# Kernel tuning notes

Hardware: AMD Instinct MI355X
Metric: run time of the kernel (lower is better)

## Reference

```python
import jax, jax.numpy as jnp
import numpy as np

B, T, D_IN = 32768, 25, 4
H = 32    # hidden_dims // 2 (per-LSTM hidden size)
HID = 64  # hidden_dims (MLP head width)
NB = 5    # number of LSTM branches
DROP = 0.4


def _lstm_layer(x_tm, Wih, Whh, b):
    # x_tm: [T, B, D] time-major. Returns all hidden states [T, B, H].
    Bn = x_tm.shape[1]
    h0 = jnp.zeros((Bn, H), x_tm.dtype)

    def step(carry, xt):
        h, c = carry
        gates = xt @ Wih.T + h @ Whh.T + b  # [B, 4H], torch gate order i,f,g,o
        i, f, g, o = jnp.split(gates, 4, axis=-1)
        c = jax.nn.sigmoid(f) * c + jax.nn.sigmoid(i) * jnp.tanh(g)
        h = jax.nn.sigmoid(o) * jnp.tanh(c)
        return (h, c), h

    (_, _), hs = jax.lax.scan(step, (h0, h0), x_tm)
    return hs


def setup_inputs() -> dict:
    key = jax.random.key(0)
    ks = jax.random.split(key, 16)
    s = 1.0 / np.sqrt(H)  # torch LSTM/Linear uniform bound scale
    u = lambda k, shape: jax.random.uniform(k, shape, jnp.float32, -s, s)
    return {
        "x": jax.random.normal(ks[0], (B, T, D_IN), jnp.float32),
        "mask": (jax.random.uniform(ks[1], (B, T, D_IN)) > DROP).astype(jnp.float32),
        # layer 0 of each of the 5 LSTMs (input D_IN -> H)
        "Wih0": u(ks[2], (NB, 4 * H, D_IN)),
        "Whh0": u(ks[3], (NB, 4 * H, H)),
        "bih0": u(ks[4], (NB, 4 * H)),
        "bhh0": u(ks[5], (NB, 4 * H)),
        # layer 1 of each of the 5 LSTMs (H -> H)
        "Wih1": u(ks[6], (NB, 4 * H, H)),
        "Whh1": u(ks[7], (NB, 4 * H, H)),
        "bih1": u(ks[8], (NB, 4 * H)),
        "bhh1": u(ks[9], (NB, 4 * H)),
        # MLP head: Linear(H->HID), GELU, Linear(HID->HID)
        "W1": u(ks[10], (HID, H)),
        "b1": u(ks[11], (HID,)),
        "W2": u(ks[12], (HID, HID)),
        "b2": u(ks[13], (HID,)),
    }


def reference(x, mask, Wih0, Whh0, bih0, bhh0, Wih1, Whh1, bih1, bhh1, W1, b1, W2, b2):
    xm = x * mask  # elementwise input dropout-mask (precomputed binary mask)
    hiddens = []
    for i in range(NB):  # fixed small structural loop over 5 distinct LSTMs
        sub = xm[:, -(i + 1) * 5 :, :]           # [B, 5*(i+1), D_IN]
        sub_tm = jnp.swapaxes(sub, 0, 1)         # time-major [t, B, D_IN]
        hs0 = _lstm_layer(sub_tm, Wih0[i], Whh0[i], bih0[i] + bhh0[i])  # [t,B,H]
        hs1 = _lstm_layer(hs0, Wih1[i], Whh1[i], bih1[i] + bhh1[i])     # [t,B,H]
        hiddens.append(hs1[-1])                  # last-layer final hidden [B,H]
    hidden = jnp.stack(hiddens, axis=1)          # [B, 5, H]
    h = jax.nn.gelu(hidden @ W1.T + b1, approximate=False)  # torch exact GELU
    out = h @ W2.T + b2                          # [B, 5, HID]
    return out
```

## Files before the change

### kernel.cpp

```cpp
#include <hip/hip_runtime.h>
#include <hip/hip_bf16.h>

#define BQ   32768
#define TT   25
#define DIN  4
#define HH   32
#define GG   128
#define NBR  5
#define HIDD 64
#define LOG2E    1.4426950408889634f
#define TWOLOG2E 2.8853900817779268f

using bfrag = __attribute__((ext_vector_type(8))) short;
using accf  = __attribute__((ext_vector_type(4))) float;

__device__ __forceinline__ float fexp2(float x){
#if __has_builtin(__builtin_amdgcn_exp2f)
  return __builtin_amdgcn_exp2f(x);
#else
  return exp2f(x);
#endif
}
__device__ __forceinline__ float frcpf(float x){
#if __has_builtin(__builtin_amdgcn_rcpf)
  return __builtin_amdgcn_rcpf(x);
#else
  return 1.0f / x;
#endif
}
__device__ __forceinline__ unsigned short fb(float f){
  unsigned u = __builtin_bit_cast(unsigned, f);
  u += 0x7fffu + ((u >> 16) & 1u);
  return (unsigned short)(u >> 16);
}
__device__ __forceinline__ bfrag pack8s(const float* p, float s){
  bfrag w;
#pragma unroll
  for (int j = 0; j < 8; ++j) w[j] = (short)fb(p[j] * s);
  return w;
}
__device__ __forceinline__ accf mma(bfrag a, bfrag b, accf c){
  return __builtin_amdgcn_mfma_f32_16x16x32_bf16(a, b, c, 0, 0, 0);
}
__device__ __forceinline__ float cellh(float iv, float fv, float gv, float ov, float& cs){
  float ei = fexp2(-iv), ef = fexp2(-fv), t = fexp2(gv);
  float r2 = frcpf(1.0f + ef);
  float r1 = frcpf((1.0f + ei) * (t + 1.0f));
  float cp = cs * r2 + ((t - 1.0f) * r1) * TWOLOG2E;
  cs = cp;
  float eo = fexp2(-ov), tc = fexp2(cp);
  float r3 = frcpf((1.0f + eo) * (tc + 1.0f));
  return (tc - 1.0f) * r3;
}

#define LDSW 4032

__global__ __launch_bounds__(64, 2) void lstm_kernel(
    const float* __restrict__ x,    const float* __restrict__ mask,
    const float* __restrict__ Wih0, const float* __restrict__ Whh0,
    const float* __restrict__ bih0, const float* __restrict__ bhh0,
    const float* __restrict__ Wih1, const float* __restrict__ Whh1,
    const float* __restrict__ bih1, const float* __restrict__ bhh1,
    const float* __restrict__ W1,   const float* __restrict__ b1,
    const float* __restrict__ W2,   const float* __restrict__ b2,
    float* __restrict__ out)
{
  __shared__ __align__(16) unsigned short smem[2 * LDSW];
  const int lane = threadIdx.x & 63;
  const int col  = lane & 15, quad = lane >> 4;
  const int tp     = blockIdx.x & 1023;
  const int branch = 4 - (int)(blockIdx.x >> 10);
  const int L = (branch + 1) * 5, t0 = TT - L;

  for (int i = lane; i < 800; i += 64) {
    int b = i / 25;
    int j = i - b * 25;
    size_t go = (size_t)(tp * 32 + b) * 100 + j * 4;
    float4 xv = *reinterpret_cast<const float4*>(x + go);
    float4 mv = *reinterpret_cast<const float4*>(mask + go);
    ushort4 sv;
    sv.x = fb(xv.x * mv.x); sv.y = fb(xv.y * mv.y);
    sv.z = fb(xv.z * mv.z); sv.w = fb(xv.w * mv.w);
    *reinterpret_cast<ushort4*>(smem + (b >> 4) * LDSW + (b & 15) * 100 + j * 4) = sv;
  }

  const float* Wih0p = Wih0 + branch * GG * DIN;
  const float* Whh0p = Whh0 + branch * GG * HH;
  const float* Wih1p = Wih1 + branch * GG * HH;
  const float* Whh1p = Whh1 + branch * GG * HH;
  const float* bi0p = bih0 + branch * GG;
  const float* bh0p = bhh0 + branch * GG;
  const float* bi1p = bih1 + branch * GG;
  const float* bh1p = bhh1 + branch * GG;

  bfrag Bx0[8], Bh0[8], Bi1[8], Bh1[8];
  float bias1[8];
#pragma unroll
  for (int nt = 0; nt < 8; ++nt) {
    const int g = nt * 16 + col;
    const float sc = (nt == 4 || nt == 5) ? TWOLOG2E : LOG2E;
    bias1[nt] = (bi1p[g] + bh1p[g]) * sc;
    Bh0[nt] = pack8s(Whh0p + g * HH + quad * 8, sc);
    Bi1[nt] = pack8s(Wih1p + g * HH + quad * 8, sc);
    Bh1[nt] = pack8s(Whh1p + g * HH + quad * 8, sc);
    bfrag bx = {0,0,0,0,0,0,0,0};
    if (quad == 0) {
      const float* q = Wih0p + g * DIN;
      bx[0] = (short)fb(q[0] * sc); bx[1] = (short)fb(q[1] * sc);
      bx[2] = (short)fb(q[2] * sc); bx[3] = (short)fb(q[3] * sc);
      bx[4] = (short)fb((bi0p[g] + bh0p[g]) * sc);
    }
    Bx0[nt] = bx;
  }
  __syncthreads();

  const accf zacc = {0.f, 0.f, 0.f, 0.f};
  bfrag aH0[2], aH1[2];
  accf c0[2][2], c1[2][2];
#pragma unroll
  for (int ch = 0; ch < 2; ++ch) {
    aH0[ch] = (bfrag){0,0,0,0,0,0,0,0};
    aH1[ch] = (bfrag){0,0,0,0,0,0,0,0};
    c0[ch][0] = zacc; c0[ch][1] = zacc;
    c1[ch][0] = zacc; c1[ch][1] = zacc;
  }

  for (int s = 0; s < L; ++s) {
    const int t = t0 + s;
#pragma unroll
    for (int ch = 0; ch < 2; ++ch) {
      unsigned short* xb  = smem + ch * LDSW;
      unsigned short* h0b = xb + 1600;
      accf acc[8];
      bfrag ax = {0,0,0,0,0,0,0,0};
      if (quad == 0) {
        ushort4 xv = *reinterpret_cast<const ushort4*>(xb + col * 100 + t * 4);
        ax[0] = (short)xv.x; ax[1] = (short)xv.y; ax[2] = (short)xv.z; ax[3] = (short)xv.w;
        ax[4] = (short)0x3F80;
      }
#pragma unroll
      for (int nt = 0; nt < 8; ++nt) acc[nt] = mma(ax, Bx0[nt], zacc);
#pragma unroll
      for (int nt = 0; nt < 8; ++nt) acc[nt] = mma(aH0[ch], Bh0[nt], acc[nt]);
#pragma unroll
      for (int ut = 0; ut < 2; ++ut) {
#pragma unroll
        for (int r = 0; r < 4; ++r) {
          float cv = c0[ch][ut][r];
          float h = cellh(acc[ut][r], acc[2 + ut][r], acc[4 + ut][r], acc[6 + ut][r], cv);
          c0[ch][ut][r] = cv;
          h0b[(quad * 4 + r) * 40 + ut * 16 + col] = fb(h);
        }
      }
    }
    __syncthreads();
#pragma unroll
    for (int ch = 0; ch < 2; ++ch)
      aH0[ch] = *reinterpret_cast<const bfrag*>(smem + ch * LDSW + 1600 + col * 40 + quad * 8);
#pragma unroll
    for (int ch = 0; ch < 2; ++ch) {
      unsigned short* h1b = smem + ch * LDSW + 2240;
      accf acc[8];
#pragma unroll
      for (int nt = 0; nt < 8; ++nt) acc[nt] = (accf){bias1[nt], bias1[nt], bias1[nt], bias1[nt]};
#pragma unroll
      for (int nt = 0; nt < 8; ++nt) acc[nt] = mma(aH0[ch], Bi1[nt], acc[nt]);
#pragma unroll
      for (int nt = 0; nt < 8; ++nt) acc[nt] = mma(aH1[ch], Bh1[nt], acc[nt]);
#pragma unroll
      for (int ut = 0; ut < 2; ++ut) {
#pragma unroll
        for (int r = 0; r < 4; ++r) {
          float cv = c1[ch][ut][r];
          float h = cellh(acc[ut][r], acc[2 + ut][r], acc[4 + ut][r], acc[6 + ut][r], cv);
          c1[ch][ut][r] = cv;
          h1b[(quad * 4 + r) * 40 + ut * 16 + col] = fb(h);
        }
      }
    }
    __syncthreads();
#pragma unroll
    for (int ch = 0; ch < 2; ++ch)
      aH1[ch] = *reinterpret_cast<const bfrag*>(smem + ch * LDSW + 2240 + col * 40 + quad * 8);
  }

  bfrag Bw1[4], Bw2a[4], Bw2b[4];
  float b1v[4], b2v[4];
#pragma unroll
  for (int nt = 0; nt < 4; ++nt) {
    const int n = nt * 16 + col;
    Bw1[nt]  = pack8s(W1 + n * HH + quad * 8, 1.0f);
    Bw2a[nt] = pack8s(W2 + n * HIDD + quad * 8, 1.0f);
    Bw2b[nt] = pack8s(W2 + n * HIDD + 32 + quad * 8, 1.0f);
    b1v[nt] = b1[n]; b2v[nt] = b2[n];
  }
#pragma unroll
  for (int ch = 0; ch < 2; ++ch) {
    unsigned short* fcb = smem + ch * LDSW + 2880;
    accf t1[4];
#pragma unroll
    for (int nt = 0; nt < 4; ++nt) t1[nt] = (accf){b1v[nt], b1v[nt], b1v[nt], b1v[nt]};
#pragma unroll
    for (int nt = 0; nt < 4; ++nt) t1[nt] = mma(aH1[ch], Bw1[nt], t1[nt]);
#pragma unroll
    for (int nt = 0; nt < 4; ++nt) {
#pragma unroll
      for (int r = 0; r < 4; ++r) {
        float v = t1[nt][r];
        v = 0.5f * v * (1.0f + erff(v * 0.70710678f));
        fcb[(quad * 4 + r) * 72 + nt * 16 + col] = fb(v);
      }
    }
  }
  __syncthreads();
#pragma unroll
  for (int ch = 0; ch < 2; ++ch) {
    unsigned short* fcb = smem + ch * LDSW + 2880;
    const int batch0 = tp * 32 + ch * 16;
    bfrag af0 = *reinterpret_cast<const bfrag*>(fcb + col * 72 + quad * 8);
    bfrag af1 = *reinterpret_cast<const bfrag*>(fcb + col * 72 + 32 + quad * 8);
    accf o[4];
#pragma unroll
    for (int nt = 0; nt < 4; ++nt) o[nt] = (accf){b2v[nt], b2v[nt], b2v[nt], b2v[nt]};
#pragma unroll
    for (int nt = 0; nt < 4; ++nt) {
      o[nt] = mma(af0, Bw2a[nt], o[nt]);
      o[nt] = mma(af1, Bw2b[nt], o[nt]);
    }
#pragma unroll
    for (int nt = 0; nt < 4; ++nt) {
#pragma unroll
      for (int r = 0; r < 4; ++r) {
        const int row = quad * 4 + r;
        out[(size_t)((batch0 + row) * NBR + branch) * HIDD + nt * 16 + col] = o[nt][r];
      }
    }
  }
}

extern "C" void kernel_launch(void* const* d_in, const int* in_sizes, int n_in,
                              void* d_out, int out_size, void* d_ws, size_t ws_size,
                              hipStream_t stream) {
  const float* x    = (const float*)d_in[0];
  const float* mask = (const float*)d_in[1];
  const float* Wih0 = (const float*)d_in[2];
  const float* Whh0 = (const float*)d_in[3];
  const float* bih0 = (const float*)d_in[4];
  const float* bhh0 = (const float*)d_in[5];
  const float* Wih1 = (const float*)d_in[6];
  const float* Whh1 = (const float*)d_in[7];
  const float* bih1 = (const float*)d_in[8];
  const float* bhh1 = (const float*)d_in[9];
  const float* W1   = (const float*)d_in[10];
  const float* b1   = (const float*)d_in[11];
  const float* W2   = (const float*)d_in[12];
  const float* b2   = (const float*)d_in[13];
  float* out = (float*)d_out;

  const int nblocks = (BQ / 32) * NBR;
  lstm_kernel<<<nblocks, 64, 0, stream>>>(x, mask, Wih0, Whh0, bih0, bhh0,
                                          Wih1, Whh1, bih1, bhh1, W1, b1, W2, b2, out);
}
```

Before: 302.9 us.

## Share LSTM weights in LDS across four waves, one 16-row tile per wave

Recurrent and input weights move from per-wave registers into shared LDS, read by four waves per block, each owning a single 16-row batch tile. Each wave now syncs only through its own LDS region, which removes the per-step block barriers, and x*mask is loaded straight from global with a one-step prefetch instead of being staged in LDS. This frees many VGPRs so more waves fit per CU, at the cost of extra LDS reads for the B fragments on every timestep. Each wave also loses the interleaving of two independent chunks that previously helped hide MFMA and transcendental latency.

```diff
diff --git a/kernel.cpp b/kernel.cpp
--- a/kernel.cpp
+++ b/kernel.cpp
@@ -8,6 +8,7 @@
 #define GG   128
 #define NBR  5
 #define HIDD 64
+#define WPB  4
 #define LOG2E    1.4426950408889634f
 #define TWOLOG2E 2.8853900817779268f
 
@@ -53,9 +54,9 @@
   return (tc - 1.0f) * r3;
 }
 
-#define LDSW 4032
-
-__global__ __launch_bounds__(64, 2) void lstm_kernel(
+#define SMEM_SH 18432
+
+__global__ __launch_bounds__(256, 3) void lstm_kernel(
     const float* __restrict__ x,    const float* __restrict__ mask,
     const float* __restrict__ Wih0, const float* __restrict__ Whh0,
     const float* __restrict__ bih0, const float* __restrict__ bhh0,
@@ -65,177 +66,162 @@
     const float* __restrict__ W2,   const float* __restrict__ b2,
     float* __restrict__ out)
 {
-  __shared__ __align__(16) unsigned short smem[2 * LDSW];
-  const int lane = threadIdx.x & 63;
+  __shared__ __align__(16) unsigned short smem[SMEM_SH];
+  unsigned short* wB = smem;
+  unsigned short* wX = smem + 12288;
+  const int tid  = threadIdx.x;
+  const int wave = tid >> 6, lane = tid & 63;
   const int col  = lane & 15, quad = lane >> 4;
-  const int tp     = blockIdx.x & 1023;
-  const int branch = 4 - (int)(blockIdx.x >> 10);
+  const int branch = 4 - (int)(blockIdx.x >> 9);
+  const int tile   = (int)(blockIdx.x & 511) * WPB + wave;
+  const int batch0 = tile * 16;
   const int L = (branch + 1) * 5, t0 = TT - L;
-
-  for (int i = lane; i < 800; i += 64) {
-    int b = i / 25;
-    int j = i - b * 25;
-    size_t go = (size_t)(tp * 32 + b) * 100 + j * 4;
-    float4 xv = *reinterpret_cast<const float4*>(x + go);
-    float4 mv = *reinterpret_cast<const float4*>(mask + go);
-    ushort4 sv;
-    sv.x = fb(xv.x * mv.x); sv.y = fb(xv.y * mv.y);
-    sv.z = fb(xv.z * mv.z); sv.w = fb(xv.w * mv.w);
-    *reinterpret_cast<ushort4*>(smem + (b >> 4) * LDSW + (b & 15) * 100 + j * 4) = sv;
-  }
-
-  const float* Wih0p = Wih0 + branch * GG * DIN;
-  const float* Whh0p = Whh0 + branch * GG * HH;
-  const float* Wih1p = Wih1 + branch * GG * HH;
-  const float* Whh1p = Whh1 + branch * GG * HH;
-  const float* bi0p = bih0 + branch * GG;
-  const float* bh0p = bhh0 + branch * GG;
-  const float* bi1p = bih1 + branch * GG;
-  const float* bh1p = bhh1 + branch * GG;
-
-  bfrag Bx0[8], Bh0[8], Bi1[8], Bh1[8];
+  unsigned short* hb = smem + 13312 + wave * 1280;
+
+  {
+    const float* srcs[3] = { Whh0 + branch * GG * HH,
+                             Wih1 + branch * GG * HH,
+                             Whh1 + branch * GG * HH };
+#pragma unroll
+    for (int m = 0; m < 3; ++m) {
+      const float* src = srcs[m];
+#pragma unroll
+      for (int i = 0; i < 16; ++i) {
+        int v = tid + i * 256;
+        float f = src[v];
+        int g = v >> 5, k = v & 31;
+        float sc = ((g >> 5) == 2) ? TWOLOG2E : LOG2E;
+        int nt = g >> 4, cv = g & 15, q = k >> 3, j = k & 7;
+        wB[((m * 8 + nt) * 64 + q * 16 + cv) * 8 + j] = fb(f * sc);
+      }
+    }
+    if (tid < 128) {
+      int nt = tid >> 4, cv = tid & 15, g = nt * 16 + cv;
+      float sc = ((g >> 5) == 2) ? TWOLOG2E : LOG2E;
+      const float* q4 = Wih0 + branch * GG * DIN + g * DIN;
+      unsigned short* d = wX + tid * 8;
+      d[0] = fb(q4[0] * sc); d[1] = fb(q4[1] * sc);
+      d[2] = fb(q4[2] * sc); d[3] = fb(q4[3] * sc);
+      d[4] = fb((bih0[branch * GG + g] + bhh0[branch * GG + g]) * sc);
+      d[5] = 0; d[6] = 0; d[7] = 0;
+    }
+  }
   float bias1[8];
 #pragma unroll
   for (int nt = 0; nt < 8; ++nt) {
-    const int g = nt * 16 + col;
-    const float sc = (nt == 4 || nt == 5) ? TWOLOG2E : LOG2E;
-    bias1[nt] = (bi1p[g] + bh1p[g]) * sc;
-    Bh0[nt] = pack8s(Whh0p + g * HH + quad * 8, sc);
-    Bi1[nt] = pack8s(Wih1p + g * HH + quad * 8, sc);
-    Bh1[nt] = pack8s(Whh1p + g * HH + quad * 8, sc);
-    bfrag bx = {0,0,0,0,0,0,0,0};
+    int g = nt * 16 + col;
+    float sc = ((g >> 5) == 2) ? TWOLOG2E : LOG2E;
+    bias1[nt] = (bih1[branch * GG + g] + bhh1[branch * GG + g]) * sc;
+  }
+  __syncthreads();
+
+  const accf zacc = {0.f, 0.f, 0.f, 0.f};
+  bfrag aH0 = {0,0,0,0,0,0,0,0}, aH1 = {0,0,0,0,0,0,0,0};
+  accf c0[2] = {zacc, zacc}, c1[2] = {zacc, zacc};
+
+  const float* xrow = x    + (size_t)(batch0 + col) * (TT * DIN);
+  const float* mrow = mask + (size_t)(batch0 + col) * (TT * DIN);
+  float4 xv, mv;
+  if (quad == 0) {
+    xv = *reinterpret_cast<const float4*>(xrow + t0 * 4);
+    mv = *reinterpret_cast<const float4*>(mrow + t0 * 4);
+  }
+
+  for (int s = 0; s < L; ++s) {
+    bfrag ax = {0,0,0,0,0,0,0,0};
     if (quad == 0) {
-      const float* q = Wih0p + g * DIN;
-      bx[0] = (short)fb(q[0] * sc); bx[1] = (short)fb(q[1] * sc);
-      bx[2] = (short)fb(q[2] * sc); bx[3] = (short)fb(q[3] * sc);
-      bx[4] = (short)fb((bi0p[g] + bh0p[g]) * sc);
-    }
-    Bx0[nt] = bx;
-  }
-  __syncthreads();
-
-  const accf zacc = {0.f, 0.f, 0.f, 0.f};
-  bfrag aH0[2], aH1[2];
-  accf c0[2][2], c1[2][2];
-#pragma unroll
-  for (int ch = 0; ch < 2; ++ch) {
-    aH0[ch] = (bfrag){0,0,0,0,0,0,0,0};
-    aH1[ch] = (bfrag){0,0,0,0,0,0,0,0};
-    c0[ch][0] = zacc; c0[ch][1] = zacc;
-    c1[ch][0] = zacc; c1[ch][1] = zacc;
-  }
-
-  for (int s = 0; s < L; ++s) {
-    const int t = t0 + s;
-#pragma unroll
-    for (int ch = 0; ch < 2; ++ch) {
-      unsigned short* xb  = smem + ch * LDSW;
-      unsigned short* h0b = xb + 1600;
-      accf acc[8];
-      bfrag ax = {0,0,0,0,0,0,0,0};
-      if (quad == 0) {
-        ushort4 xv = *reinterpret_cast<const ushort4*>(xb + col * 100 + t * 4);
-        ax[0] = (short)xv.x; ax[1] = (short)xv.y; ax[2] = (short)xv.z; ax[3] = (short)xv.w;
-        ax[4] = (short)0x3F80;
-      }
-#pragma unroll
-      for (int nt = 0; nt < 8; ++nt) acc[nt] = mma(ax, Bx0[nt], zacc);
-#pragma unroll
-      for (int nt = 0; nt < 8; ++nt) acc[nt] = mma(aH0[ch], Bh0[nt], acc[nt]);
-#pragma unroll
-      for (int ut = 0; ut < 2; ++ut) {
-#pragma unroll
-        for (int r = 0; r < 4; ++r) {
-          float cv = c0[ch][ut][r];
-          float h = cellh(acc[ut][r], acc[2 + ut][r], acc[4 + ut][r], acc[6 + ut][r], cv);
-          c0[ch][ut][r] = cv;
-          h0b[(quad * 4 + r) * 40 + ut * 16 + col] = fb(h);
-        }
-      }
-    }
-    __syncthreads();
-#pragma unroll
-    for (int ch = 0; ch < 2; ++ch)
-      aH0[ch] = *reinterpret_cast<const bfrag*>(smem + ch * LDSW + 1600 + col * 40 + quad * 8);
-#pragma unroll
-    for (int ch = 0; ch < 2; ++ch) {
-      unsigned short* h1b = smem + ch * LDSW + 2240;
-      accf acc[8];
-#pragma unroll
-      for (int nt = 0; nt < 8; ++nt) acc[nt] = (accf){bias1[nt], bias1[nt], bias1[nt], bias1[nt]};
-#pragma unroll
-      for (int nt = 0; nt < 8; ++nt) acc[nt] = mma(aH0[ch], Bi1[nt], acc[nt]);
-#pragma unroll
-      for (int nt = 0; nt < 8; ++nt) acc[nt] = mma(aH1[ch], Bh1[nt], acc[nt]);
-#pragma unroll
-      for (int ut = 0; ut < 2; ++ut) {
-#pragma unroll
-        for (int r = 0; r < 4; ++r) {
-          float cv = c1[ch][ut][r];
-          float h = cellh(acc[ut][r], acc[2 + ut][r], acc[4 + ut][r], acc[6 + ut][r], cv);
-          c1[ch][ut][r] = cv;
-          h1b[(quad * 4 + r) * 40 + ut * 16 + col] = fb(h);
-        }
-      }
-    }
-    __syncthreads();
-#pragma unroll
-    for (int ch = 0; ch < 2; ++ch)
-      aH1[ch] = *reinterpret_cast<const bfrag*>(smem + ch * LDSW + 2240 + col * 40 + quad * 8);
-  }
-
-  bfrag Bw1[4], Bw2a[4], Bw2b[4];
-  float b1v[4], b2v[4];
-#pragma unroll
-  for (int nt = 0; nt < 4; ++nt) {
-    const int n = nt * 16 + col;
-    Bw1[nt]  = pack8s(W1 + n * HH + quad * 8, 1.0f);
-    Bw2a[nt] = pack8s(W2 + n * HIDD + quad * 8, 1.0f);
-    Bw2b[nt] = pack8s(W2 + n * HIDD + 32 + quad * 8, 1.0f);
-    b1v[nt] = b1[n]; b2v[nt] = b2[n];
-  }
-#pragma unroll
-  for (int ch = 0; ch < 2; ++ch) {
-    unsigned short* fcb = smem + ch * LDSW + 2880;
+      ax[0] = (short)fb(xv.x * mv.x); ax[1] = (short)fb(xv.y * mv.y);
+      ax[2] = (short)fb(xv.z * mv.z); ax[3] = (short)fb(xv.w * mv.w);
+      ax[4] = (short)0x3F80;
+      if (s + 1 < L) {
+        xv = *reinterpret_cast<const float4*>(xrow + (t0 + s + 1) * 4);
+        mv = *reinterpret_cast<const float4*>(mrow + (t0 + s + 1) * 4);
+      }
+    }
+    accf acc[8];
+#pragma unroll
+    for (int nt = 0; nt < 8; ++nt) {
+      bfrag bx = {0,0,0,0,0,0,0,0};
+      if (quad == 0) bx = *reinterpret_cast<const bfrag*>(wX + (nt * 16 + col) * 8);
+      acc[nt] = mma(ax, bx, zacc);
+    }
+#pragma unroll
+    for (int nt = 0; nt < 8; ++nt) {
+      bfrag bw = *reinterpret_cast<const bfrag*>(wB + ((0 * 8 + nt) * 64 + quad * 16 + col) * 8);
+      acc[nt] = mma(aH0, bw, acc[nt]);
+    }
+#pragma unroll
+    for (int ut = 0; ut < 2; ++ut)
+#pragma unroll
+      for (int r = 0; r < 4; ++r) {
+        float cv = c0[ut][r];
+        float h = cellh(acc[ut][r], acc[2 + ut][r], acc[4 + ut][r], acc[6 + ut][r], cv);
+        c0[ut][r] = cv;
+        hb[(quad * 4 + r) * 40 + ut * 16 + col] = fb(h);
+      }
+    aH0 = *reinterpret_cast<const bfrag*>(hb + col * 40 + quad * 8);
+#pragma unroll
+    for (int nt = 0; nt < 8; ++nt) acc[nt] = (accf){bias1[nt], bias1[nt], bias1[nt], bias1[nt]};
+#pragma unroll
+    for (int nt = 0; nt < 8; ++nt) {
+      bfrag bw = *reinterpret_cast<const bfrag*>(wB + ((1 * 8 + nt) * 64 + quad * 16 + col) * 8);
+      acc[nt] = mma(aH0, bw, acc[nt]);
+    }
+#pragma unroll
+    for (int nt = 0; nt < 8; ++nt) {
+      bfrag bw = *reinterpret_cast<const bfrag*>(wB + ((2 * 8 + nt) * 64 + quad * 16 + col) * 8);
+      acc[nt] = mma(aH1, bw, acc[nt]);
+    }
+#pragma unroll
+    for (int ut = 0; ut < 2; ++ut)
+#pragma unroll
+      for (int r = 0; r < 4; ++r) {
+        float cv = c1[ut][r];
+        float h = cellh(acc[ut][r], acc[2 + ut][r], acc[4 + ut][r], acc[6 + ut][r], cv);
+        c1[ut][r] = cv;
+        hb[640 + (quad * 4 + r) * 40 + ut * 16 + col] = fb(h);
+      }
+    aH1 = *reinterpret_cast<const bfrag*>(hb + 640 + col * 40 + quad * 8);
+  }
+
+  unsigned short* fcb = hb;
+  {
     accf t1[4];
 #pragma unroll
-    for (int nt = 0; nt < 4; ++nt) t1[nt] = (accf){b1v[nt], b1v[nt], b1v[nt], b1v[nt]};
-#pragma unroll
-    for (int nt = 0; nt < 4; ++nt) t1[nt] = mma(aH1[ch], Bw1[nt], t1[nt]);
-#pragma unroll
     for (int nt = 0; nt < 4; ++nt) {
+      const int n = nt * 16 + col;
+      bfrag bw1 = pack8s(W1 + n * HH + quad * 8, 1.0f);
+      t1[nt] = (accf){b1[n], b1[n], b1[n], b1[n]};
+      t1[nt] = mma(aH1, bw1, t1[nt]);
+    }
+#pragma unroll
+    for (int nt = 0; nt < 4; ++nt)
 #pragma unroll
       for (int r = 0; r < 4; ++r) {
         float v = t1[nt][r];
         v = 0.5f * v * (1.0f + erff(v * 0.70710678f));
         fcb[(quad * 4 + r) * 72 + nt * 16 + col] = fb(v);
       }
-    }
-  }
-  __syncthreads();
-#pragma unroll
-  for (int ch = 0; ch < 2; ++ch) {
-    unsigned short* fcb = smem + ch * LDSW + 2880;
-    const int batch0 = tp * 32 + ch * 16;
-    bfrag af0 = *reinterpret_cast<const bfrag*>(fcb + col * 72 + quad * 8);
-    bfrag af1 = *reinterpret_cast<const bfrag*>(fcb + col * 72 + 32 + quad * 8);
-    accf o[4];
-#pragma unroll
-    for (int nt = 0; nt < 4; ++nt) o[nt] = (accf){b2v[nt], b2v[nt], b2v[nt], b2v[nt]};
-#pragma unroll
-    for (int nt = 0; nt < 4; ++nt) {
-      o[nt] = mma(af0, Bw2a[nt], o[nt]);
-      o[nt] = mma(af1, Bw2b[nt], o[nt]);
-    }
-#pragma unroll
-    for (int nt = 0; nt < 4; ++nt) {
-#pragma unroll
-      for (int r = 0; r < 4; ++r) {
-        const int row = quad * 4 + r;
-        out[(size_t)((batch0 + row) * NBR + branch) * HIDD + nt * 16 + col] = o[nt][r];
-      }
-    }
-  }
+  }
+  bfrag af0 = *reinterpret_cast<const bfrag*>(fcb + col * 72 + quad * 8);
+  bfrag af1 = *reinterpret_cast<const bfrag*>(fcb + col * 72 + 32 + quad * 8);
+  accf o[4];
+#pragma unroll
+  for (int nt = 0; nt < 4; ++nt) {
+    const int n = nt * 16 + col;
+    bfrag bw2a = pack8s(W2 + n * HIDD + quad * 8, 1.0f);
+    bfrag bw2b = pack8s(W2 + n * HIDD + 32 + quad * 8, 1.0f);
+    o[nt] = (accf){b2[n], b2[n], b2[n], b2[n]};
+    o[nt] = mma(af0, bw2a, o[nt]);
+    o[nt] = mma(af1, bw2b, o[nt]);
+  }
+#pragma unroll
+  for (int nt = 0; nt < 4; ++nt)
+#pragma unroll
+    for (int r = 0; r < 4; ++r) {
+      const int row = quad * 4 + r;
+      out[(size_t)((batch0 + row) * NBR + branch) * HIDD + nt * 16 + col] = o[nt][r];
+    }
 }
 
 extern "C" void kernel_launch(void* const* d_in, const int* in_sizes, int n_in,
@@ -257,7 +243,7 @@
   const float* b2   = (const float*)d_in[13];
   float* out = (float*)d_out;
 
-  const int nblocks = (BQ / 32) * NBR;
-  lstm_kernel<<<nblocks, 64, 0, stream>>>(x, mask, Wih0, Whh0, bih0, bhh0,
-                                          Wih1, Whh1, bih1, bhh1, W1, b1, W2, b2, out);
-}
+  const int nblocks = (BQ / (16 * WPB)) * NBR;
+  lstm_kernel<<<nblocks, 256, 0, stream>>>(x, mask, Wih0, Whh0, bih0, bhh0,
+                                           Wih1, Whh1, bih1, bhh1, W1, b1, W2, b2, out);
+}
```

New measurement: 284.7 us. 6.0% less time.
